# Kernel optimization log

Measured on AMD Instinct MI355X. Metric: run time of the kernel, lower is better.

The kernel has to match this reference:

```python
import jax, jax.numpy as jnp
import numpy as np

# ---- static configuration (mirrors resource grid / pilot pattern) ----
NB_SYMB = 14                 # num_ofdm_symbols
NSC = 4096                   # fft_size == num_effective_subcarriers (dc_null=False)
PILOT_SYMBS = np.array([2, 11], dtype=np.int32)  # OFDM symbols carrying pilots
STEP = 2                     # subcarriers_step (comb-2, offset 0)
M = NSC // STEP              # pilots per pilot OFDM symbol (constant, as asserted)
BATCH = 512
SC = np.arange(0, NSC, STEP, dtype=np.int32)     # pilot subcarrier positions
ROWS = np.repeat(PILOT_SYMBS, M)                 # flattened pilot (symbol, sc) map,
COLS = np.tile(SC, len(PILOT_SYMBS))             # frequency-then-time ordering


def _time_interp_tables():
    """Replicates _generate_time_interpolation_index_ with numpy (static)."""
    u = PILOT_SYMBS
    idx = np.empty((2, NB_SYMB), dtype=np.int32)
    nf = np.empty(NB_SYMB, dtype=np.float32)
    if u[0] != 0:
        idx[:, : u[0]] = u[0]
        nf[: u[0]] = 0.0
    idx[:, u[-1]:] = u[-1]
    nf[u[-1]:] = 0.0
    for i in range(len(u) - 1):
        idx[0, u[i]: u[i + 1]] = u[i]
        idx[1, u[i]: u[i + 1]] = u[i + 1]
        d = u[i + 1] - u[i]
        nf[u[i]: u[i + 1]] = np.arange(d, dtype=np.float32) / d
    return idx[0], idx[1], nf

IDX0, IDX1, NORM = _time_interp_tables()


def setup_inputs() -> dict:
    key = jax.random.key(0)
    k1, k2 = jax.random.split(key)
    shape = (BATCH, len(PILOT_SYMBS) * M)
    return {
        "h_pilots_real": jax.random.normal(k1, shape, dtype=jnp.float32),
        "h_pilots_imag": jax.random.normal(k2, shape, dtype=jnp.float32),
    }


def reference(h_pilots_real, h_pilots_imag):
    pilots = (h_pilots_real + 1j * h_pilots_imag).astype(jnp.complex64)  # [B, P]
    B = pilots.shape[0]
    # scatter_nd of pilot estimates into the full grid [T, F, B]
    updates = pilots.T  # [P, B]
    grid = jnp.zeros((NB_SYMB, NSC, B), jnp.complex64).at[ROWS, COLS].set(updates)
    # gather pilot OFDM symbols then pilot subcarriers -> [S, M, B]
    est_pilots = grid[PILOT_SYMBS][:, SC, :]
    # M-point unitary DFT along frequency (sionna.signal.fft is ortho-normalized)
    dft = jnp.fft.fft(est_pilots, axis=1, norm="ortho")
    # constant cutoff: fc = floor(M/2)
    fc = M // 2
    padded = jnp.concatenate(
        [
            dft[:, :fc, :],
            jnp.zeros((len(PILOT_SYMBS), NSC - 2 * fc, B), jnp.complex64),
            dft[:, -fc:, :],
        ],
        axis=1,
    )  # [S, NSC, B]
    scaling = jnp.asarray(np.sqrt(np.float32(STEP)), dtype=jnp.complex64)
    freq_interp = scaling * jnp.fft.ifft(padded, axis=1, norm="ortho")
    # scatter interpolated pilot symbols back into the time grid
    interp = jnp.zeros((NB_SYMB, NSC, B), jnp.complex64).at[PILOT_SYMBS].set(freq_interp)
    # time-domain linear interpolation: (H[m+1]-H[m]) * l/L + H[m]
    h0 = interp[IDX0]  # [T, F, B]
    h1 = interp[IDX1]
    norm = jnp.asarray(NORM)[:, None, None]
    out = (h1 - h0) * norm + h0
    # -> [batch, num_ofdm_symbols, num_subcarriers]
    return jnp.transpose(out, (2, 0, 1))
```

## Files before the change

kernel.cpp:

```cpp
#include <hip/hip_runtime.h>
#include <math.h>


#define NSC  4096
#define PI_F 3.14159265358979323846f
#define RSQ2 0.70710678118654752f

__device__ __forceinline__ int pada(int i) { return i + 2 * (i >> 5); }

__device__ __forceinline__ void bf_fwd(float2& a, float2& c, float tc, float ts) {
  const float tx = a.x - c.x, ty = a.y - c.y;
  a.x += c.x; a.y += c.y;
  c.x = tx * tc - ty * ts;
  c.y = tx * ts + ty * tc;
}
__device__ __forceinline__ void bf_inv(float2& a, float2& c, float tc, float ts) {
  const float tx = c.x * tc - c.y * ts, ty = c.x * ts + c.y * tc;
  c.x = a.x - tx; c.y = a.y - ty;
  a.x += tx; a.y += ty;
}

__device__ __forceinline__ void fwd3(float2* x, float c, float s) {
  bf_fwd(x[0], x[4], c, -s);
  { const float cj = RSQ2 * (c - s), sj = RSQ2 * (c + s);
    bf_fwd(x[1], x[5], cj, -sj); }
  bf_fwd(x[2], x[6], -s, -c);
  { const float cj = -RSQ2 * (s + c), sj = RSQ2 * (c - s);
    bf_fwd(x[3], x[7], cj, -sj); }
  const float c2 = c * c - s * s, s2 = 2.f * c * s;
  bf_fwd(x[0], x[2], c2, -s2);  bf_fwd(x[4], x[6], c2, -s2);
  bf_fwd(x[1], x[3], -s2, -c2); bf_fwd(x[5], x[7], -s2, -c2);
  const float c4 = c2 * c2 - s2 * s2, s4 = 2.f * c2 * s2;
  bf_fwd(x[0], x[1], c4, -s4); bf_fwd(x[2], x[3], c4, -s4);
  bf_fwd(x[4], x[5], c4, -s4); bf_fwd(x[6], x[7], c4, -s4);
}

__device__ __forceinline__ void inv3(float2* x, float c, float s) {
  const float c2 = c * c - s * s, s2 = 2.f * c * s;
  const float c4 = c2 * c2 - s2 * s2, s4 = 2.f * c2 * s2;
  bf_inv(x[0], x[1], c4, s4); bf_inv(x[2], x[3], c4, s4);
  bf_inv(x[4], x[5], c4, s4); bf_inv(x[6], x[7], c4, s4);
  bf_inv(x[0], x[2], c2, s2);  bf_inv(x[4], x[6], c2, s2);
  bf_inv(x[1], x[3], -s2, c2); bf_inv(x[5], x[7], -s2, c2);
  bf_inv(x[0], x[4], c, s);
  { const float cj = RSQ2 * (c - s), sj = RSQ2 * (c + s);
    bf_inv(x[1], x[5], cj, sj); }
  bf_inv(x[2], x[6], -s, c);
  { const float cj = -RSQ2 * (s + c), sj = RSQ2 * (c - s);
    bf_inv(x[3], x[7], cj, sj); }
}

__global__ __launch_bounds__(256)
void tdi_pk(const float* __restrict__ in_r,
            const float* __restrict__ in_i,
            float4* __restrict__ out) {
  __shared__ __align__(16) float2 As[2176];
  __shared__ float sred[4][4];

  const int u = threadIdx.x;
  const int b = blockIdx.x;

  const float* __restrict__ pr0 = in_r + ((size_t)b << 12);
  const float* __restrict__ pr1 = pr0 + 2048;
  const float* __restrict__ pi0 = in_i + ((size_t)b << 12);
  const float* __restrict__ pi1 = pi0 + 2048;

  float2 x[8];
  float s, c;

  float a_r0 = 0.f, a_r1 = 0.f, a_i0 = 0.f, a_i1 = 0.f;
#pragma unroll
  for (int j = 0; j < 8; ++j) {
    const int n = u + 256 * j;
    x[j] = make_float2(pr0[n], pr1[n]);
    a_r0 += x[j].x;  a_r1 += x[j].y;
    a_i0 += pi0[n];  a_i1 += pi1[n];
  }
  {
    const float sg = (u & 1) ? -1.f : 1.f;
    a_r0 *= sg; a_r1 *= sg; a_i0 *= sg; a_i1 *= sg;
#pragma unroll
    for (int off = 32; off >= 1; off >>= 1) {
      a_r0 += __shfl_xor(a_r0, off, 64);
      a_r1 += __shfl_xor(a_r1, off, 64);
      a_i0 += __shfl_xor(a_i0, off, 64);
      a_i1 += __shfl_xor(a_i1, off, 64);
    }
    if ((u & 63) == 0) {
      const int w = u >> 6;
      sred[w][0] = a_r0; sred[w][1] = a_r1;
      sred[w][2] = a_i0; sred[w][3] = a_i1;
    }
  }
  __sincosf((float)u * (PI_F / 1024.f), &s, &c);
  fwd3(x, c, s);
#pragma unroll
  for (int j = 0; j < 8; ++j) As[pada(u + 256 * j)] = x[j];
  __syncthreads();

  {
    const int q = u & 31;
    const int base = ((u >> 5) << 8) | q;
#pragma unroll
    for (int j = 0; j < 8; ++j) x[j] = As[pada(base + 32 * j)];
    __sincosf((float)q * (PI_F / 128.f), &s, &c);
    fwd3(x, c, s);
#pragma unroll
    for (int j = 0; j < 8; ++j) As[pada(base + 32 * j)] = x[j];
  }
  __syncthreads();

  {
    const int q = u & 3;
    const int base = ((u >> 2) << 5) | q;
#pragma unroll
    for (int j = 0; j < 8; ++j) x[j] = As[pada(base + 4 * j)];
    __sincosf((float)q * (PI_F / 16.f), &s, &c);
    fwd3(x, c, s);
#pragma unroll
    for (int j = 0; j < 8; ++j) As[pada(base + 4 * j)] = x[j];
  }
  __syncthreads();

  {
    const int base = u << 3;
#pragma unroll
    for (int j = 0; j < 8; ++j) x[j] = As[pada(base + j)];
#pragma unroll
    for (int g = 0; g < 8; g += 4) {
      float2 t;
      t.x = x[g].x - x[g+2].x;  t.y = x[g].y - x[g+2].y;
      x[g].x += x[g+2].x;       x[g].y += x[g+2].y;
      x[g+2] = t;
      t.x = x[g+1].x - x[g+3].x; t.y = x[g+1].y - x[g+3].y;
      x[g+1].x += x[g+3].x;      x[g+1].y += x[g+3].y;
      x[g+3] = make_float2(t.y, -t.x);
    }
#pragma unroll
    for (int g = 0; g < 8; g += 2) {
      float2 t;
      t.x = x[g].x - x[g+1].x; t.y = x[g].y - x[g+1].y;
      x[g].x += x[g+1].x;      x[g].y += x[g+1].y;
      x[g+1] = t;
    }
    {
      const float c8[8] = { 1.f,  0.92387953f,  0.70710678f,  0.38268343f,
                            0.f, -0.38268343f, -0.70710678f, -0.92387953f };
      const float s8[8] = { 0.f,  0.38268343f,  0.70710678f,  0.92387953f,
                            1.f,  0.92387953f,  0.70710678f,  0.38268343f };
      float cp, sp;
      __sincosf((float)(__brev((unsigned)u) >> 24) * (PI_F / 2048.f), &sp, &cp);
#pragma unroll
      for (int j = 0; j < 8; ++j) {
        const int rv = ((j & 1) << 2) | (j & 2) | (j >> 2);
        const float sc = (j & 1) ? -(1.f / 2048.f) : (1.f / 2048.f);
        const float fc = (cp * c8[rv] - sp * s8[rv]) * sc;
        const float fs = (sp * c8[rv] + cp * s8[rv]) * sc;
        const float2 a = x[j];
        x[j] = make_float2(a.x * fc - a.y * fs, a.x * fs + a.y * fc);
      }
    }
#pragma unroll
    for (int g = 0; g < 8; g += 2) {
      const float2 t = x[g+1];
      x[g+1].x = x[g].x - t.x; x[g+1].y = x[g].y - t.y;
      x[g].x  += t.x;          x[g].y  += t.y;
    }
#pragma unroll
    for (int g = 0; g < 8; g += 4) {
      float2 t = x[g+2];
      x[g+2].x = x[g].x - t.x; x[g+2].y = x[g].y - t.y;
      x[g].x  += t.x;          x[g].y  += t.y;
      t = make_float2(-x[g+3].y, x[g+3].x);
      x[g+3].x = x[g+1].x - t.x; x[g+3].y = x[g+1].y - t.y;
      x[g+1].x += t.x;           x[g+1].y += t.y;
    }
#pragma unroll
    for (int j = 0; j < 8; ++j) As[pada(base + j)] = x[j];
  }
  __syncthreads();

  {
    const int q = u & 3;
    const int base = ((u >> 2) << 5) | q;
#pragma unroll
    for (int j = 0; j < 8; ++j) x[j] = As[pada(base + 4 * j)];
    __sincosf((float)q * (PI_F / 16.f), &s, &c);
    inv3(x, c, s);
#pragma unroll
    for (int j = 0; j < 8; ++j) As[pada(base + 4 * j)] = x[j];
  }
  __syncthreads();

  {
    const int q = u & 31;
    const int base = ((u >> 5) << 8) | q;
#pragma unroll
    for (int j = 0; j < 8; ++j) x[j] = As[pada(base + 32 * j)];
    __sincosf((float)q * (PI_F / 128.f), &s, &c);
    inv3(x, c, s);
#pragma unroll
    for (int j = 0; j < 8; ++j) As[pada(base + 32 * j)] = x[j];
  }
  __syncthreads();

  {
#pragma unroll
    for (int j = 0; j < 8; ++j) x[j] = As[pada(u + 256 * j)];
    __sincosf((float)u * (PI_F / 1024.f), &s, &c);
    inv3(x, c, s);
#pragma unroll
    for (int j = 0; j < 8; ++j) As[pada(u + 256 * j)] = x[j];
  }
  __syncthreads();

  const float S0r = sred[0][0] + sred[1][0] + sred[2][0] + sred[3][0];
  const float S1r = sred[0][1] + sred[1][1] + sred[2][1] + sred[3][1];
  const float S0i = sred[0][2] + sred[1][2] + sred[2][2] + sred[3][2];
  const float S1i = sred[0][3] + sred[1][3] + sred[2][3] + sred[3][3];
  const float alpha = (S0i - S1r) * (1.f / 2048.f);
  const float beta  = (S0r + S1i) * (1.f / 2048.f);

  float4* __restrict__ orow = out + (size_t)b * (14 * 1024);
#pragma unroll
  for (int e = 0; e < 4; ++e) {
    const int q = u + (e << 8);
    const float2 E0 = *(const float2*)&pr0[2 * q];
    const float2 E1 = *(const float2*)&pr1[2 * q];
    const float4 a  = *(const float4*)&As[pada(2 * q)];
    const float2 O0 = make_float2(a.x + alpha, a.z - alpha);
    const float2 O1 = make_float2(a.y + beta,  a.w - beta);
#pragma unroll
    for (int t = 0; t < 14; ++t) {
      const float wt = (t < 2) ? 0.f : (t >= 11) ? 1.f : (float)(t - 2) * (1.f / 9.f);
      float4 v;
      v.x = E0.x + wt * (E1.x - E0.x);
      v.y = O0.x + wt * (O1.x - O0.x);
      v.z = E0.y + wt * (E1.y - E0.y);
      v.w = O0.y + wt * (O1.y - O0.y);
      orow[t * 1024 + q] = v;
    }
  }
}

extern "C" void kernel_launch(void* const* d_in, const int* in_sizes, int n_in,
                              void* d_out, int out_size, void* d_ws, size_t ws_size,
                              hipStream_t stream) {
  const float* hr = (const float*)d_in[0];
  const float* hi = (const float*)d_in[1];
  const int batch = in_sizes[0] / NSC;
  tdi_pk<<<dim3(batch), dim3(256), 0, stream>>>(hr, hi, (float4*)d_out);
}
```

Measured before the change: 134.0 us.

## Process two batch rows per block to increase ILP and halve grid size

Each block now computes the FFT pipeline for two batch entries at once, interleaving their butterflies and sharing twiddle computations and barriers. The middle radix stage is also changed to use float4 shared-memory loads and stores. The aim is more independent work per thread to hide LDS and sync latency and to amortize twiddle math. The costs are double the shared memory and more registers per block, and a grid of only 256 blocks on a GPU with 256 CUs, which may reduce latency hiding in this output-write-bound kernel.

```diff
diff --git a/kernel.cpp b/kernel.cpp
--- a/kernel.cpp
+++ b/kernel.cpp
@@ -50,63 +50,136 @@
     bf_inv(x[3], x[7], cj, sj); }
 }
 
+__device__ __forceinline__ void mid4(float2* x, float cp, float sp) {
+  const float c8[8] = { 1.f,  0.92387953f,  0.70710678f,  0.38268343f,
+                        0.f, -0.38268343f, -0.70710678f, -0.92387953f };
+  const float s8[8] = { 0.f,  0.38268343f,  0.70710678f,  0.92387953f,
+                        1.f,  0.92387953f,  0.70710678f,  0.38268343f };
+#pragma unroll
+  for (int g = 0; g < 8; g += 4) {
+    float2 t;
+    t.x = x[g].x - x[g+2].x;  t.y = x[g].y - x[g+2].y;
+    x[g].x += x[g+2].x;       x[g].y += x[g+2].y;
+    x[g+2] = t;
+    t.x = x[g+1].x - x[g+3].x; t.y = x[g+1].y - x[g+3].y;
+    x[g+1].x += x[g+3].x;      x[g+1].y += x[g+3].y;
+    x[g+3] = make_float2(t.y, -t.x);
+  }
+#pragma unroll
+  for (int g = 0; g < 8; g += 2) {
+    float2 t;
+    t.x = x[g].x - x[g+1].x; t.y = x[g].y - x[g+1].y;
+    x[g].x += x[g+1].x;      x[g].y += x[g+1].y;
+    x[g+1] = t;
+  }
+#pragma unroll
+  for (int j = 0; j < 8; ++j) {
+    const int rv = ((j & 1) << 2) | (j & 2) | (j >> 2);
+    const float sc = (j & 1) ? -(1.f / 2048.f) : (1.f / 2048.f);
+    const float fc = (cp * c8[rv] - sp * s8[rv]) * sc;
+    const float fs = (sp * c8[rv] + cp * s8[rv]) * sc;
+    const float2 a = x[j];
+    x[j] = make_float2(a.x * fc - a.y * fs, a.x * fs + a.y * fc);
+  }
+#pragma unroll
+  for (int g = 0; g < 8; g += 2) {
+    const float2 t = x[g+1];
+    x[g+1].x = x[g].x - t.x; x[g+1].y = x[g].y - t.y;
+    x[g].x  += t.x;          x[g].y  += t.y;
+  }
+#pragma unroll
+  for (int g = 0; g < 8; g += 4) {
+    float2 t = x[g+2];
+    x[g+2].x = x[g].x - t.x; x[g+2].y = x[g].y - t.y;
+    x[g].x  += t.x;          x[g].y  += t.y;
+    t = make_float2(-x[g+3].y, x[g+3].x);
+    x[g+3].x = x[g+1].x - t.x; x[g+3].y = x[g+1].y - t.y;
+    x[g+1].x += t.x;           x[g+1].y += t.y;
+  }
+}
+
 __global__ __launch_bounds__(256)
-void tdi_pk(const float* __restrict__ in_r,
-            const float* __restrict__ in_i,
-            float4* __restrict__ out) {
-  __shared__ __align__(16) float2 As[2176];
-  __shared__ float sred[4][4];
+void tdi_dual(const float* __restrict__ in_r,
+              const float* __restrict__ in_i,
+              float4* __restrict__ out,
+              int batch) {
+  __shared__ __align__(16) float2 As[2][2176];
+  __shared__ float sred[2][4][4];
 
   const int u = threadIdx.x;
-  const int b = blockIdx.x;
-
-  const float* __restrict__ pr0 = in_r + ((size_t)b << 12);
-  const float* __restrict__ pr1 = pr0 + 2048;
-  const float* __restrict__ pi0 = in_i + ((size_t)b << 12);
-  const float* __restrict__ pi1 = pi0 + 2048;
-
-  float2 x[8];
+  const int g = blockIdx.x;
+  const int bA = 2 * g;
+  const int bB = (2 * g + 1 < batch) ? 2 * g + 1 : 2 * g;
+
+  const float* __restrict__ prA0 = in_r + ((size_t)bA << 12);
+  const float* __restrict__ prA1 = prA0 + 2048;
+  const float* __restrict__ piA0 = in_i + ((size_t)bA << 12);
+  const float* __restrict__ piA1 = piA0 + 2048;
+  const float* __restrict__ prB0 = in_r + ((size_t)bB << 12);
+  const float* __restrict__ prB1 = prB0 + 2048;
+  const float* __restrict__ piB0 = in_i + ((size_t)bB << 12);
+  const float* __restrict__ piB1 = piB0 + 2048;
+
+  float2 xA[8], xB[8];
   float s, c;
 
-  float a_r0 = 0.f, a_r1 = 0.f, a_i0 = 0.f, a_i1 = 0.f;
-#pragma unroll
-  for (int j = 0; j < 8; ++j) {
-    const int n = u + 256 * j;
-    x[j] = make_float2(pr0[n], pr1[n]);
-    a_r0 += x[j].x;  a_r1 += x[j].y;
-    a_i0 += pi0[n];  a_i1 += pi1[n];
-  }
-  {
+  {
+    float aAr0 = 0.f, aAr1 = 0.f, aAi0 = 0.f, aAi1 = 0.f;
+    float aBr0 = 0.f, aBr1 = 0.f, aBi0 = 0.f, aBi1 = 0.f;
+#pragma unroll
+    for (int j = 0; j < 8; ++j) {
+      const int n = u + 256 * j;
+      xA[j] = make_float2(prA0[n], prA1[n]);
+      xB[j] = make_float2(prB0[n], prB1[n]);
+      aAr0 += xA[j].x;  aAr1 += xA[j].y;
+      aBr0 += xB[j].x;  aBr1 += xB[j].y;
+      aAi0 += piA0[n];  aAi1 += piA1[n];
+      aBi0 += piB0[n];  aBi1 += piB1[n];
+    }
     const float sg = (u & 1) ? -1.f : 1.f;
-    a_r0 *= sg; a_r1 *= sg; a_i0 *= sg; a_i1 *= sg;
+    aAr0 *= sg; aAr1 *= sg; aAi0 *= sg; aAi1 *= sg;
+    aBr0 *= sg; aBr1 *= sg; aBi0 *= sg; aBi1 *= sg;
 #pragma unroll
     for (int off = 32; off >= 1; off >>= 1) {
-      a_r0 += __shfl_xor(a_r0, off, 64);
-      a_r1 += __shfl_xor(a_r1, off, 64);
-      a_i0 += __shfl_xor(a_i0, off, 64);
-      a_i1 += __shfl_xor(a_i1, off, 64);
+      aAr0 += __shfl_xor(aAr0, off, 64);  aAr1 += __shfl_xor(aAr1, off, 64);
+      aAi0 += __shfl_xor(aAi0, off, 64);  aAi1 += __shfl_xor(aAi1, off, 64);
+      aBr0 += __shfl_xor(aBr0, off, 64);  aBr1 += __shfl_xor(aBr1, off, 64);
+      aBi0 += __shfl_xor(aBi0, off, 64);  aBi1 += __shfl_xor(aBi1, off, 64);
     }
     if ((u & 63) == 0) {
       const int w = u >> 6;
-      sred[w][0] = a_r0; sred[w][1] = a_r1;
-      sred[w][2] = a_i0; sred[w][3] = a_i1;
-    }
-  }
-  __sincosf((float)u * (PI_F / 1024.f), &s, &c);
-  fwd3(x, c, s);
-#pragma unroll
-  for (int j = 0; j < 8; ++j) As[pada(u + 256 * j)] = x[j];
+      sred[0][w][0] = aAr0; sred[0][w][1] = aAr1;
+      sred[0][w][2] = aAi0; sred[0][w][3] = aAi1;
+      sred[1][w][0] = aBr0; sred[1][w][1] = aBr1;
+      sred[1][w][2] = aBi0; sred[1][w][3] = aBi1;
+    }
+    __sincosf((float)u * (PI_F / 1024.f), &s, &c);
+    fwd3(xA, c, s);
+    fwd3(xB, c, s);
+#pragma unroll
+    for (int j = 0; j < 8; ++j) {
+      As[0][pada(u + 256 * j)] = xA[j];
+      As[1][pada(u + 256 * j)] = xB[j];
+    }
+  }
   __syncthreads();
 
   {
     const int q = u & 31;
     const int base = ((u >> 5) << 8) | q;
 #pragma unroll
-    for (int j = 0; j < 8; ++j) x[j] = As[pada(base + 32 * j)];
+    for (int j = 0; j < 8; ++j) {
+      xA[j] = As[0][pada(base + 32 * j)];
+      xB[j] = As[1][pada(base + 32 * j)];
+    }
     __sincosf((float)q * (PI_F / 128.f), &s, &c);
-    fwd3(x, c, s);
-#pragma unroll
-    for (int j = 0; j < 8; ++j) As[pada(base + 32 * j)] = x[j];
+    fwd3(xA, c, s);
+    fwd3(xB, c, s);
+#pragma unroll
+    for (int j = 0; j < 8; ++j) {
+      As[0][pada(base + 32 * j)] = xA[j];
+      As[1][pada(base + 32 * j)] = xB[j];
+    }
   }
   __syncthreads();
 
@@ -114,69 +187,41 @@
     const int q = u & 3;
     const int base = ((u >> 2) << 5) | q;
 #pragma unroll
-    for (int j = 0; j < 8; ++j) x[j] = As[pada(base + 4 * j)];
+    for (int j = 0; j < 8; ++j) {
+      xA[j] = As[0][pada(base + 4 * j)];
+      xB[j] = As[1][pada(base + 4 * j)];
+    }
     __sincosf((float)q * (PI_F / 16.f), &s, &c);
-    fwd3(x, c, s);
-#pragma unroll
-    for (int j = 0; j < 8; ++j) As[pada(base + 4 * j)] = x[j];
+    fwd3(xA, c, s);
+    fwd3(xB, c, s);
+#pragma unroll
+    for (int j = 0; j < 8; ++j) {
+      As[0][pada(base + 4 * j)] = xA[j];
+      As[1][pada(base + 4 * j)] = xB[j];
+    }
   }
   __syncthreads();
 
   {
     const int base = u << 3;
 #pragma unroll
-    for (int j = 0; j < 8; ++j) x[j] = As[pada(base + j)];
-#pragma unroll
-    for (int g = 0; g < 8; g += 4) {
-      float2 t;
-      t.x = x[g].x - x[g+2].x;  t.y = x[g].y - x[g+2].y;
-      x[g].x += x[g+2].x;       x[g].y += x[g+2].y;
-      x[g+2] = t;
-      t.x = x[g+1].x - x[g+3].x; t.y = x[g+1].y - x[g+3].y;
-      x[g+1].x += x[g+3].x;      x[g+1].y += x[g+3].y;
-      x[g+3] = make_float2(t.y, -t.x);
-    }
-#pragma unroll
-    for (int g = 0; g < 8; g += 2) {
-      float2 t;
-      t.x = x[g].x - x[g+1].x; t.y = x[g].y - x[g+1].y;
-      x[g].x += x[g+1].x;      x[g].y += x[g+1].y;
-      x[g+1] = t;
-    }
-    {
-      const float c8[8] = { 1.f,  0.92387953f,  0.70710678f,  0.38268343f,
-                            0.f, -0.38268343f, -0.70710678f, -0.92387953f };
-      const float s8[8] = { 0.f,  0.38268343f,  0.70710678f,  0.92387953f,
-                            1.f,  0.92387953f,  0.70710678f,  0.38268343f };
-      float cp, sp;
-      __sincosf((float)(__brev((unsigned)u) >> 24) * (PI_F / 2048.f), &sp, &cp);
-#pragma unroll
-      for (int j = 0; j < 8; ++j) {
-        const int rv = ((j & 1) << 2) | (j & 2) | (j >> 2);
-        const float sc = (j & 1) ? -(1.f / 2048.f) : (1.f / 2048.f);
-        const float fc = (cp * c8[rv] - sp * s8[rv]) * sc;
-        const float fs = (sp * c8[rv] + cp * s8[rv]) * sc;
-        const float2 a = x[j];
-        x[j] = make_float2(a.x * fc - a.y * fs, a.x * fs + a.y * fc);
-      }
-    }
-#pragma unroll
-    for (int g = 0; g < 8; g += 2) {
-      const float2 t = x[g+1];
-      x[g+1].x = x[g].x - t.x; x[g+1].y = x[g].y - t.y;
-      x[g].x  += t.x;          x[g].y  += t.y;
-    }
-#pragma unroll
-    for (int g = 0; g < 8; g += 4) {
-      float2 t = x[g+2];
-      x[g+2].x = x[g].x - t.x; x[g+2].y = x[g].y - t.y;
-      x[g].x  += t.x;          x[g].y  += t.y;
-      t = make_float2(-x[g+3].y, x[g+3].x);
-      x[g+3].x = x[g+1].x - t.x; x[g+3].y = x[g+1].y - t.y;
-      x[g+1].x += t.x;           x[g+1].y += t.y;
-    }
-#pragma unroll
-    for (int j = 0; j < 8; ++j) As[pada(base + j)] = x[j];
+    for (int k = 0; k < 4; ++k) {
+      const float4 a = *(const float4*)&As[0][pada(base + 2 * k)];
+      const float4 b = *(const float4*)&As[1][pada(base + 2 * k)];
+      xA[2*k]   = make_float2(a.x, a.y);  xA[2*k+1] = make_float2(a.z, a.w);
+      xB[2*k]   = make_float2(b.x, b.y);  xB[2*k+1] = make_float2(b.z, b.w);
+    }
+    float cp, sp;
+    __sincosf((float)(__brev((unsigned)u) >> 24) * (PI_F / 2048.f), &sp, &cp);
+    mid4(xA, cp, sp);
+    mid4(xB, cp, sp);
+#pragma unroll
+    for (int k = 0; k < 4; ++k) {
+      *(float4*)&As[0][pada(base + 2 * k)] =
+          make_float4(xA[2*k].x, xA[2*k].y, xA[2*k+1].x, xA[2*k+1].y);
+      *(float4*)&As[1][pada(base + 2 * k)] =
+          make_float4(xB[2*k].x, xB[2*k].y, xB[2*k+1].x, xB[2*k+1].y);
+    }
   }
   __syncthreads();
 
@@ -184,11 +229,18 @@
     const int q = u & 3;
     const int base = ((u >> 2) << 5) | q;
 #pragma unroll
-    for (int j = 0; j < 8; ++j) x[j] = As[pada(base + 4 * j)];
+    for (int j = 0; j < 8; ++j) {
+      xA[j] = As[0][pada(base + 4 * j)];
+      xB[j] = As[1][pada(base + 4 * j)];
+    }
     __sincosf((float)q * (PI_F / 16.f), &s, &c);
-    inv3(x, c, s);
-#pragma unroll
-    for (int j = 0; j < 8; ++j) As[pada(base + 4 * j)] = x[j];
+    inv3(xA, c, s);
+    inv3(xB, c, s);
+#pragma unroll
+    for (int j = 0; j < 8; ++j) {
+      As[0][pada(base + 4 * j)] = xA[j];
+      As[1][pada(base + 4 * j)] = xB[j];
+    }
   }
   __syncthreads();
 
@@ -196,49 +248,69 @@
     const int q = u & 31;
     const int base = ((u >> 5) << 8) | q;
 #pragma unroll
-    for (int j = 0; j < 8; ++j) x[j] = As[pada(base + 32 * j)];
+    for (int j = 0; j < 8; ++j) {
+      xA[j] = As[0][pada(base + 32 * j)];
+      xB[j] = As[1][pada(base + 32 * j)];
+    }
     __sincosf((float)q * (PI_F / 128.f), &s, &c);
-    inv3(x, c, s);
-#pragma unroll
-    for (int j = 0; j < 8; ++j) As[pada(base + 32 * j)] = x[j];
-  }
-  __syncthreads();
-
-  {
-#pragma unroll
-    for (int j = 0; j < 8; ++j) x[j] = As[pada(u + 256 * j)];
+    inv3(xA, c, s);
+    inv3(xB, c, s);
+#pragma unroll
+    for (int j = 0; j < 8; ++j) {
+      As[0][pada(base + 32 * j)] = xA[j];
+      As[1][pada(base + 32 * j)] = xB[j];
+    }
+  }
+  __syncthreads();
+
+  {
+#pragma unroll
+    for (int j = 0; j < 8; ++j) {
+      xA[j] = As[0][pada(u + 256 * j)];
+      xB[j] = As[1][pada(u + 256 * j)];
+    }
     __sincosf((float)u * (PI_F / 1024.f), &s, &c);
-    inv3(x, c, s);
-#pragma unroll
-    for (int j = 0; j < 8; ++j) As[pada(u + 256 * j)] = x[j];
-  }
-  __syncthreads();
-
-  const float S0r = sred[0][0] + sred[1][0] + sred[2][0] + sred[3][0];
-  const float S1r = sred[0][1] + sred[1][1] + sred[2][1] + sred[3][1];
-  const float S0i = sred[0][2] + sred[1][2] + sred[2][2] + sred[3][2];
-  const float S1i = sred[0][3] + sred[1][3] + sred[2][3] + sred[3][3];
-  const float alpha = (S0i - S1r) * (1.f / 2048.f);
-  const float beta  = (S0r + S1i) * (1.f / 2048.f);
-
-  float4* __restrict__ orow = out + (size_t)b * (14 * 1024);
-#pragma unroll
-  for (int e = 0; e < 4; ++e) {
-    const int q = u + (e << 8);
-    const float2 E0 = *(const float2*)&pr0[2 * q];
-    const float2 E1 = *(const float2*)&pr1[2 * q];
-    const float4 a  = *(const float4*)&As[pada(2 * q)];
-    const float2 O0 = make_float2(a.x + alpha, a.z - alpha);
-    const float2 O1 = make_float2(a.y + beta,  a.w - beta);
-#pragma unroll
-    for (int t = 0; t < 14; ++t) {
-      const float wt = (t < 2) ? 0.f : (t >= 11) ? 1.f : (float)(t - 2) * (1.f / 9.f);
-      float4 v;
-      v.x = E0.x + wt * (E1.x - E0.x);
-      v.y = O0.x + wt * (O1.x - O0.x);
-      v.z = E0.y + wt * (E1.y - E0.y);
-      v.w = O0.y + wt * (O1.y - O0.y);
-      orow[t * 1024 + q] = v;
+    inv3(xA, c, s);
+    inv3(xB, c, s);
+#pragma unroll
+    for (int j = 0; j < 8; ++j) {
+      As[0][pada(u + 256 * j)] = xA[j];
+      As[1][pada(u + 256 * j)] = xB[j];
+    }
+  }
+  __syncthreads();
+
+#pragma unroll
+  for (int f = 0; f < 2; ++f) {
+    const int b = (f == 0) ? bA : bB;
+    const float S0r = sred[f][0][0] + sred[f][1][0] + sred[f][2][0] + sred[f][3][0];
+    const float S1r = sred[f][0][1] + sred[f][1][1] + sred[f][2][1] + sred[f][3][1];
+    const float S0i = sred[f][0][2] + sred[f][1][2] + sred[f][2][2] + sred[f][3][2];
+    const float S1i = sred[f][0][3] + sred[f][1][3] + sred[f][2][3] + sred[f][3][3];
+    const float alpha = (S0i - S1r) * (1.f / 2048.f);
+    const float beta  = (S0r + S1i) * (1.f / 2048.f);
+
+    const float* __restrict__ p0 = in_r + ((size_t)b << 12);
+    const float* __restrict__ p1 = p0 + 2048;
+    float4* __restrict__ orow = out + (size_t)b * (14 * 1024);
+#pragma unroll
+    for (int e = 0; e < 4; ++e) {
+      const int q = u + (e << 8);
+      const float2 E0 = *(const float2*)&p0[2 * q];
+      const float2 E1 = *(const float2*)&p1[2 * q];
+      const float4 a  = *(const float4*)&As[f][pada(2 * q)];
+      const float2 O0 = make_float2(a.x + alpha, a.z - alpha);
+      const float2 O1 = make_float2(a.y + beta,  a.w - beta);
+#pragma unroll
+      for (int t = 0; t < 14; ++t) {
+        const float wt = (t < 2) ? 0.f : (t >= 11) ? 1.f : (float)(t - 2) * (1.f / 9.f);
+        float4 v;
+        v.x = E0.x + wt * (E1.x - E0.x);
+        v.y = O0.x + wt * (O1.x - O0.x);
+        v.z = E0.y + wt * (E1.y - E0.y);
+        v.w = O0.y + wt * (O1.y - O0.y);
+        orow[t * 1024 + q] = v;
+      }
     }
   }
 }
@@ -249,5 +321,6 @@
   const float* hr = (const float*)d_in[0];
   const float* hi = (const float*)d_in[1];
   const int batch = in_sizes[0] / NSC;
-  tdi_pk<<<dim3(batch), dim3(256), 0, stream>>>(hr, hi, (float4*)d_out);
-}
+  const int nblk = (batch + 1) / 2;
+  tdi_dual<<<dim3(nblk), dim3(256), 0, stream>>>(hr, hi, (float4*)d_out, batch);
+}
```

Measured after the change: 135.0 us. About the same (+0.8%).
